# Optimization experiments

Hardware: AMD Instinct MI355X
Metric: run time of the kernel (lower is better)

Reference implementation:

```python
import jax, jax.numpy as jnp
import numpy as np
from jax import lax

MAXV = 8      # convex intersection of two quads has at most 8 vertices
EPS = 1e-7
LOSS_WEIGHT = 1.0


def _edge_cross(A, B, P):
    # z of (B-A) x (P-A); >= 0 means P is on the left of directed edge A->B (inside for CCW poly)
    return (B[0] - A[0]) * (P[1] - A[1]) - (B[1] - A[1]) * (P[0] - A[0])


def _clip_halfplane(pts, n, A, B):
    # Sutherland-Hodgman clip of polygon pts[:n] against left halfplane of edge A->B.
    # pts: (MAXV,2) buffer, n: traced vertex count. Returns new buffer + count.
    def body(i, carry):
        out, m = carry
        valid = i < n
        cur = pts[i]
        nxt = pts[jnp.mod(i + 1, jnp.maximum(n, 1))]
        dc = _edge_cross(A, B, cur)
        dn = _edge_cross(A, B, nxt)
        denom = dc - dn
        t = dc / jnp.where(jnp.abs(denom) < EPS, 1.0, denom)
        ip = cur + t * (nxt - cur)
        add_cur = valid & (dc >= 0)
        idx = jnp.minimum(m, MAXV - 1)
        out = jnp.where(add_cur, out.at[idx].set(cur), out)
        m = m + add_cur.astype(jnp.int32)
        add_ip = valid & jnp.logical_xor(dc >= 0, dn >= 0)
        idx = jnp.minimum(m, MAXV - 1)
        out = jnp.where(add_ip, out.at[idx].set(ip), out)
        m = m + add_ip.astype(jnp.int32)
        return out, m
    out0 = jnp.zeros((MAXV, 2), pts.dtype)
    return lax.fori_loop(0, MAXV, body, (out0, jnp.int32(0)))


def _shoelace_masked(pts, n):
    # signed area of pts[:n] (fixed-size loop, masked)
    def body(i, acc):
        valid = i < n
        cur = pts[i]
        nxt = pts[jnp.mod(i + 1, jnp.maximum(n, 1))]
        term = cur[0] * nxt[1] - cur[1] * nxt[0]
        return acc + jnp.where(valid, term, jnp.zeros((), pts.dtype))
    return 0.5 * lax.fori_loop(0, MAXV, body, jnp.zeros((), pts.dtype))


def _quad_signed_area(p):  # p: (4,2)
    x, y = p[:, 0], p[:, 1]
    return 0.5 * jnp.sum(x * jnp.roll(y, -1) - y * jnp.roll(x, -1))


def _diou_single(p, t):
    # p, t: (4,2) quads -> scalar poly DIoU loss (a=0 => standard DIoU penalty)
    sa_p = _quad_signed_area(p)
    sa_t = _quad_signed_area(t)
    p = jnp.where(sa_p < 0, p[::-1], p)   # force CCW orientation
    t = jnp.where(sa_t < 0, t[::-1], t)
    area_p = jnp.abs(sa_p)
    area_t = jnp.abs(sa_t)
    # clip p by the 4 halfplanes of t
    buf = jnp.zeros((MAXV, 2), p.dtype).at[:4].set(p)
    n = jnp.int32(4)
    for k in range(4):
        buf, n = _clip_halfplane(buf, n, t[k], t[(k + 1) % 4])
    inter = jnp.abs(_shoelace_masked(buf, n))
    union = area_p + area_t - inter
    iou = inter / (union + EPS)
    cp = p.mean(0)
    ct = t.mean(0)
    d2 = jnp.sum((cp - ct) ** 2)
    allp = jnp.concatenate([p, t], axis=0)
    c2 = jnp.sum((allp.max(0) - allp.min(0)) ** 2) + EPS
    return 1.0 - iou + d2 / c2


def setup_inputs() -> dict:
    key = jax.random.key(0)
    k1, k2 = jax.random.split(key)
    N = 2_000_000
    pred = jax.random.uniform(k1, (N, 8), dtype=jnp.float32)
    target = jax.random.uniform(k2, (N, 8), dtype=jnp.float32)
    return {"pred": pred, "target": target}


def reference(pred, target):
    p = pred.reshape(-1, 4, 2)
    t = target.reshape(-1, 4, 2)
    losses = jax.vmap(_diou_single)(p, t)  # (N,)
    return LOSS_WEIGHT * losses.mean()
```

## Files before the change

### kernel.cpp

```cpp
#include <hip/hip_runtime.h>

#define NBLOCKS 2048
#define NTHREADS 256
#define FEPS 1e-7f

typedef __attribute__((ext_vector_type(2))) float f32x2;

__device__ __forceinline__ float frcp(float x) { return __builtin_amdgcn_rcpf(x); }

__device__ __forceinline__ float cross2(f32x2 a, f32x2 b) {
    f32x2 bs = __builtin_shufflevector(b, b, 1, 0);
    f32x2 m = a * bs;
    return m.x - m.y;
}

__device__ __forceinline__ int clip1_to_lds(f32x2* base, const f32x2 (&p)[4],
                                            float ex, float ey, float h) {
    float c[4];
#pragma unroll
    for (int j = 0; j < 4; ++j)
        c[j] = fmaf(ex, p[j].y, -fmaf(ey, p[j].x, h));
    int m = 0;
#pragma unroll
    for (int i = 0; i < 4; ++i) {
        const int ip1 = (i + 1) & 3;
        float dc = c[i], dn = c[ip1];
        f32x2 cur = p[i], nxt = p[ip1];
        float denom = dc - dn;
        float d = (fabsf(denom) < FEPS) ? 1.0f : denom;
        float t = dc * frcp(d);
        f32x2 ts = {t, t};
        f32x2 ip = __builtin_elementwise_fma(ts, nxt - cur, cur);
        bool sc = dc >= 0.0f, sn = dn >= 0.0f;

        int i1 = sc ? m : 8;
        base[i1 * NTHREADS] = cur;
        m += sc;

        bool aip = (sc != sn);
        int i2 = aip ? m : 8;
        base[i2 * NTHREADS] = ip;
        m += aip;
    }
    return m;
}

__device__ __forceinline__ int clip_lds(f32x2* base, int n,
                                        float ex, float ey, float h) {
    f32x2 v[8];
    float c[8];
#pragma unroll
    for (int j = 0; j < 8; ++j) {
        v[j] = base[j * NTHREADS];
        c[j] = fmaf(ex, v[j].y, -fmaf(ey, v[j].x, h));
    }
    int m = 0;
#pragma unroll
    for (int i = 0; i < 8; ++i) {
        if (i >= 4 && !__any(i < n)) break;
        bool valid = i < n;
        bool wrap = (i + 1 == n);
        const int ip1 = (i < 7) ? (i + 1) : 7;
        f32x2 nxt = wrap ? v[0] : v[ip1];
        float dc = c[i];
        float dn = wrap ? c[0] : c[ip1];
        f32x2 cur = v[i];
        float denom = dc - dn;
        float d = (fabsf(denom) < FEPS) ? 1.0f : denom;
        float t = dc * frcp(d);
        f32x2 ts = {t, t};
        f32x2 ip = __builtin_elementwise_fma(ts, nxt - cur, cur);
        bool sc = dc >= 0.0f, sn = dn >= 0.0f;

        bool add_cur = valid && sc;
        int i1;
        if (i < 4) i1 = add_cur ? m : 8;
        else       i1 = add_cur ? ((m < 7) ? m : 7) : 8;
        base[i1 * NTHREADS] = cur;
        m += add_cur;

        bool add_ip = valid && (sc != sn);
        int i2;
        if (i < 4) i2 = add_ip ? m : 8;
        else       i2 = add_ip ? ((m < 7) ? m : 7) : 8;
        base[i2 * NTHREADS] = ip;
        m += add_ip;
    }
    return m;
}

__device__ __forceinline__ float diou_quad(f32x2* base,
                                           float4 Pa, float4 Pb, float4 Ta, float4 Tb) {
    f32x2 p[4] = {{Pa.x, Pa.y}, {Pa.z, Pa.w}, {Pb.x, Pb.y}, {Pb.z, Pb.w}};
    f32x2 t[4] = {{Ta.x, Ta.y}, {Ta.z, Ta.w}, {Tb.x, Tb.y}, {Tb.z, Tb.w}};

    float sa_p = 0.5f * (cross2(p[0], p[1]) + cross2(p[1], p[2]) +
                         cross2(p[2], p[3]) + cross2(p[3], p[0]));
    float sa_t = 0.5f * (cross2(t[0], t[1]) + cross2(t[1], t[2]) +
                         cross2(t[2], t[3]) + cross2(t[3], t[0]));

    if (sa_p < 0.0f) {
        f32x2 w;
        w = p[0]; p[0] = p[3]; p[3] = w;
        w = p[1]; p[1] = p[2]; p[2] = w;
    }
    if (sa_t < 0.0f) {
        f32x2 w;
        w = t[0]; t[0] = t[3]; t[3] = w;
        w = t[1]; t[1] = t[2]; t[2] = w;
    }
    float area_p = fabsf(sa_p);
    float area_t = fabsf(sa_t);

    int n;
    {
        float ex = t[1].x - t[0].x, ey = t[1].y - t[0].y;
        n = clip1_to_lds(base, p, ex, ey, fmaf(ex, t[0].y, -ey * t[0].x));
    }
    {
        float ex = t[2].x - t[1].x, ey = t[2].y - t[1].y;
        n = clip_lds(base, n, ex, ey, fmaf(ex, t[1].y, -ey * t[1].x));
    }
    {
        float ex = t[3].x - t[2].x, ey = t[3].y - t[2].y;
        n = clip_lds(base, n, ex, ey, fmaf(ex, t[2].y, -ey * t[2].x));
    }
    {
        float ex = t[0].x - t[3].x, ey = t[0].y - t[3].y;
        n = clip_lds(base, n, ex, ey, fmaf(ex, t[3].y, -ey * t[3].x));
    }

    f32x2 v[8];
#pragma unroll
    for (int j = 0; j < 8; ++j) v[j] = base[j * NTHREADS];
    float acc = 0.0f;
#pragma unroll
    for (int i = 0; i < 8; ++i) {
        if (i >= 4 && !__any(i < n)) break;
        bool valid = i < n;
        bool wrap = (i + 1 == n);
        const int ip1 = (i < 7) ? (i + 1) : 7;
        f32x2 nxt = wrap ? v[0] : v[ip1];
        float term = cross2(v[i], nxt);
        acc += valid ? term : 0.0f;
    }
    float inter = fabsf(0.5f * acc);
    float uni = area_p + area_t - inter;
    float iou = inter * frcp(uni + FEPS);

    f32x2 cp = (p[0] + p[1] + p[2] + p[3]) * 0.25f;
    f32x2 ct = (t[0] + t[1] + t[2] + t[3]) * 0.25f;
    f32x2 e = cp - ct;
    f32x2 e2 = e * e;
    float d2 = e2.x + e2.y;

    f32x2 mn = __builtin_elementwise_min(
        __builtin_elementwise_min(__builtin_elementwise_min(p[0], p[1]),
                                  __builtin_elementwise_min(p[2], p[3])),
        __builtin_elementwise_min(__builtin_elementwise_min(t[0], t[1]),
                                  __builtin_elementwise_min(t[2], t[3])));
    f32x2 mx = __builtin_elementwise_max(
        __builtin_elementwise_max(__builtin_elementwise_max(p[0], p[1]),
                                  __builtin_elementwise_max(p[2], p[3])),
        __builtin_elementwise_max(__builtin_elementwise_max(t[0], t[1]),
                                  __builtin_elementwise_max(t[2], t[3])));
    f32x2 dd = mx - mn;
    f32x2 dd2 = dd * dd;
    float c2 = dd2.x + dd2.y + FEPS;

    return 1.0f - iou + d2 * frcp(c2);
}

__global__ __launch_bounds__(NTHREADS, 6) void diou_main(const float* __restrict__ pred,
                                                         const float* __restrict__ target,
                                                         double* __restrict__ partial,
                                                         int N) {
    __shared__ f32x2 poly[9 * NTHREADS];
    __shared__ double wsum[NTHREADS / 64];
    f32x2* base = &poly[threadIdx.x];

    const float4* p4 = reinterpret_cast<const float4*>(pred);
    const float4* t4 = reinterpret_cast<const float4*>(target);

    const int stride = NBLOCKS * NTHREADS;
    int i = blockIdx.x * NTHREADS + threadIdx.x;
    double acc = 0.0;
    if (i < N) {
        float4 pa = p4[2 * i], pb = p4[2 * i + 1];
        float4 ta = t4[2 * i], tb = t4[2 * i + 1];
        for (;;) {
            int inx = i + stride;
            bool has = inx < N;
            float4 npa, npb, nta, ntb;
            if (has) {
                npa = p4[2 * inx]; npb = p4[2 * inx + 1];
                nta = t4[2 * inx]; ntb = t4[2 * inx + 1];
            }
            acc += (double)diou_quad(base, pa, pb, ta, tb);
            if (!has) break;
            pa = npa; pb = npb; ta = nta; tb = ntb;
            i = inx;
        }
    }

#pragma unroll
    for (int off = 32; off > 0; off >>= 1) acc += __shfl_down(acc, off, 64);
    int lane = threadIdx.x & 63, wid = threadIdx.x >> 6;
    if (lane == 0) wsum[wid] = acc;
    __syncthreads();
    if (threadIdx.x == 0) {
        double s = 0.0;
#pragma unroll
        for (int w = 0; w < NTHREADS / 64; ++w) s += wsum[w];
        partial[blockIdx.x] = s;
    }
}

__global__ __launch_bounds__(256) void diou_finalize(const double* __restrict__ partial,
                                                     float* __restrict__ out,
                                                     int nparts, double invN) {
    __shared__ double s[256];
    double acc = 0.0;
    for (int i = threadIdx.x; i < nparts; i += 256) acc += partial[i];
    s[threadIdx.x] = acc;
    __syncthreads();
#pragma unroll
    for (int off = 128; off > 0; off >>= 1) {
        if (threadIdx.x < off) s[threadIdx.x] += s[threadIdx.x + off];
        __syncthreads();
    }
    if (threadIdx.x == 0) out[0] = (float)(s[0] * invN);
}

extern "C" void kernel_launch(void* const* d_in, const int* in_sizes, int n_in,
                              void* d_out, int out_size, void* d_ws, size_t ws_size,
                              hipStream_t stream) {
    const float* pred = (const float*)d_in[0];
    const float* target = (const float*)d_in[1];
    float* out = (float*)d_out;
    int N = in_sizes[0] / 8;

    double* partial = (double*)d_ws;

    diou_main<<<NBLOCKS, NTHREADS, 0, stream>>>(pred, target, partial, N);
    diou_finalize<<<1, 256, 0, stream>>>(partial, out, NBLOCKS, 1.0 / (double)N);
}
```

Baseline: 53.90 us.

## Fuse last clip stage with shoelace area and drop software prefetch

The fourth Sutherland-Hodgman clip now accumulates the shoelace area on the fly, tracking the previous and first emitted vertices in registers. This removes one round of LDS stores and reloads for the final polygon. The grid-stride loop also loses its manual next-iteration prefetch, which cuts register pressure but exposes load latency. cross2 becomes a single fma form.

```diff
diff --git a/kernel.cpp b/kernel.cpp
--- a/kernel.cpp
+++ b/kernel.cpp
@@ -9,9 +9,7 @@
 __device__ __forceinline__ float frcp(float x) { return __builtin_amdgcn_rcpf(x); }
 
 __device__ __forceinline__ float cross2(f32x2 a, f32x2 b) {
-    f32x2 bs = __builtin_shufflevector(b, b, 1, 0);
-    f32x2 m = a * bs;
-    return m.x - m.y;
+    return fmaf(a.x, b.y, -(a.y * b.x));
 }
 
 __device__ __forceinline__ int clip1_to_lds(f32x2* base, const f32x2 (&p)[4],
@@ -89,50 +87,17 @@
     return m;
 }
 
-__device__ __forceinline__ float diou_quad(f32x2* base,
-                                           float4 Pa, float4 Pb, float4 Ta, float4 Tb) {
-    f32x2 p[4] = {{Pa.x, Pa.y}, {Pa.z, Pa.w}, {Pb.x, Pb.y}, {Pb.z, Pb.w}};
-    f32x2 t[4] = {{Ta.x, Ta.y}, {Ta.z, Ta.w}, {Tb.x, Tb.y}, {Tb.z, Tb.w}};
-
-    float sa_p = 0.5f * (cross2(p[0], p[1]) + cross2(p[1], p[2]) +
-                         cross2(p[2], p[3]) + cross2(p[3], p[0]));
-    float sa_t = 0.5f * (cross2(t[0], t[1]) + cross2(t[1], t[2]) +
-                         cross2(t[2], t[3]) + cross2(t[3], t[0]));
-
-    if (sa_p < 0.0f) {
-        f32x2 w;
-        w = p[0]; p[0] = p[3]; p[3] = w;
-        w = p[1]; p[1] = p[2]; p[2] = w;
-    }
-    if (sa_t < 0.0f) {
-        f32x2 w;
-        w = t[0]; t[0] = t[3]; t[3] = w;
-        w = t[1]; t[1] = t[2]; t[2] = w;
-    }
-    float area_p = fabsf(sa_p);
-    float area_t = fabsf(sa_t);
-
-    int n;
-    {
-        float ex = t[1].x - t[0].x, ey = t[1].y - t[0].y;
-        n = clip1_to_lds(base, p, ex, ey, fmaf(ex, t[0].y, -ey * t[0].x));
-    }
-    {
-        float ex = t[2].x - t[1].x, ey = t[2].y - t[1].y;
-        n = clip_lds(base, n, ex, ey, fmaf(ex, t[1].y, -ey * t[1].x));
-    }
-    {
-        float ex = t[3].x - t[2].x, ey = t[3].y - t[2].y;
-        n = clip_lds(base, n, ex, ey, fmaf(ex, t[2].y, -ey * t[2].x));
-    }
-    {
-        float ex = t[0].x - t[3].x, ey = t[0].y - t[3].y;
-        n = clip_lds(base, n, ex, ey, fmaf(ex, t[3].y, -ey * t[3].x));
-    }
-
+__device__ __forceinline__ float clip4_shoelace(const f32x2* base, int n,
+                                                float ex, float ey, float h) {
     f32x2 v[8];
-#pragma unroll
-    for (int j = 0; j < 8; ++j) v[j] = base[j * NTHREADS];
+    float c[8];
+#pragma unroll
+    for (int j = 0; j < 8; ++j) {
+        v[j] = base[j * NTHREADS];
+        c[j] = fmaf(ex, v[j].y, -fmaf(ey, v[j].x, h));
+    }
+    f32x2 first = {0.0f, 0.0f}, prev = {0.0f, 0.0f};
+    int m = 0;
     float acc = 0.0f;
 #pragma unroll
     for (int i = 0; i < 8; ++i) {
@@ -141,10 +106,81 @@
         bool wrap = (i + 1 == n);
         const int ip1 = (i < 7) ? (i + 1) : 7;
         f32x2 nxt = wrap ? v[0] : v[ip1];
-        float term = cross2(v[i], nxt);
-        acc += valid ? term : 0.0f;
-    }
-    float inter = fabsf(0.5f * acc);
+        float dc = c[i];
+        float dn = wrap ? c[0] : c[ip1];
+        f32x2 cur = v[i];
+        float denom = dc - dn;
+        float d = (fabsf(denom) < FEPS) ? 1.0f : denom;
+        float t = dc * frcp(d);
+        f32x2 ts = {t, t};
+        f32x2 ip = __builtin_elementwise_fma(ts, nxt - cur, cur);
+        bool sc = dc >= 0.0f, sn = dn >= 0.0f;
+
+        bool add_cur = valid && sc;
+        {
+            float term = cross2(prev, cur);
+            acc += (add_cur && m > 0) ? term : 0.0f;
+            first = (add_cur && m == 0) ? cur : first;
+            prev = add_cur ? cur : prev;
+            m += add_cur;
+        }
+        bool add_ip = valid && (sc != sn);
+        {
+            float term = cross2(prev, ip);
+            acc += (add_ip && m > 0) ? term : 0.0f;
+            first = (add_ip && m == 0) ? ip : first;
+            prev = add_ip ? ip : prev;
+            m += add_ip;
+        }
+    }
+    float closing = cross2(prev, first);
+    acc += (m > 0) ? closing : 0.0f;
+    return acc;
+}
+
+__device__ __forceinline__ float diou_quad(f32x2* base,
+                                           float4 Pa, float4 Pb, float4 Ta, float4 Tb) {
+    f32x2 p[4] = {{Pa.x, Pa.y}, {Pa.z, Pa.w}, {Pb.x, Pb.y}, {Pb.z, Pb.w}};
+    f32x2 t[4] = {{Ta.x, Ta.y}, {Ta.z, Ta.w}, {Tb.x, Tb.y}, {Tb.z, Tb.w}};
+
+    float sa_p = 0.5f * (cross2(p[0], p[1]) + cross2(p[1], p[2]) +
+                         cross2(p[2], p[3]) + cross2(p[3], p[0]));
+    float sa_t = 0.5f * (cross2(t[0], t[1]) + cross2(t[1], t[2]) +
+                         cross2(t[2], t[3]) + cross2(t[3], t[0]));
+
+    if (sa_p < 0.0f) {
+        f32x2 w;
+        w = p[0]; p[0] = p[3]; p[3] = w;
+        w = p[1]; p[1] = p[2]; p[2] = w;
+    }
+    if (sa_t < 0.0f) {
+        f32x2 w;
+        w = t[0]; t[0] = t[3]; t[3] = w;
+        w = t[1]; t[1] = t[2]; t[2] = w;
+    }
+    float area_p = fabsf(sa_p);
+    float area_t = fabsf(sa_t);
+
+    int n;
+    {
+        float ex = t[1].x - t[0].x, ey = t[1].y - t[0].y;
+        n = clip1_to_lds(base, p, ex, ey, fmaf(ex, t[0].y, -ey * t[0].x));
+    }
+    {
+        float ex = t[2].x - t[1].x, ey = t[2].y - t[1].y;
+        n = clip_lds(base, n, ex, ey, fmaf(ex, t[1].y, -ey * t[1].x));
+    }
+    {
+        float ex = t[3].x - t[2].x, ey = t[3].y - t[2].y;
+        n = clip_lds(base, n, ex, ey, fmaf(ex, t[2].y, -ey * t[2].x));
+    }
+    float sl;
+    {
+        float ex = t[0].x - t[3].x, ey = t[0].y - t[3].y;
+        sl = clip4_shoelace(base, n, ex, ey, fmaf(ex, t[3].y, -ey * t[3].x));
+    }
+
+    float inter = fabsf(0.5f * sl);
     float uni = area_p + area_t - inter;
     float iou = inter * frcp(uni + FEPS);
 
@@ -182,25 +218,11 @@
     const float4* p4 = reinterpret_cast<const float4*>(pred);
     const float4* t4 = reinterpret_cast<const float4*>(target);
 
-    const int stride = NBLOCKS * NTHREADS;
-    int i = blockIdx.x * NTHREADS + threadIdx.x;
     double acc = 0.0;
-    if (i < N) {
+    for (int i = blockIdx.x * NTHREADS + threadIdx.x; i < N; i += NBLOCKS * NTHREADS) {
         float4 pa = p4[2 * i], pb = p4[2 * i + 1];
         float4 ta = t4[2 * i], tb = t4[2 * i + 1];
-        for (;;) {
-            int inx = i + stride;
-            bool has = inx < N;
-            float4 npa, npb, nta, ntb;
-            if (has) {
-                npa = p4[2 * inx]; npb = p4[2 * inx + 1];
-                nta = t4[2 * inx]; ntb = t4[2 * inx + 1];
-            }
-            acc += (double)diou_quad(base, pa, pb, ta, tb);
-            if (!has) break;
-            pa = npa; pb = npb; ta = nta; tb = ntb;
-            i = inx;
-        }
+        acc += (double)diou_quad(base, pa, pb, ta, tb);
     }
 
 #pragma unroll
```

Result: faster. 52.61 us (-2.4%).
